# Optimization experiments

Measured on AMD Instinct MI355X. Metric: run time of the kernel, lower is better.

## Reference

```python
import jax, jax.numpy as jnp
import numpy as np

B, T, E = 2, 2048, 1024
H, D = 8, 512
ROPE_BASE = 10000.0


def apply_rope(x):
    # x: [B, H, T, D] -- rotary positional embedding, half-split convention
    t = x.shape[2]
    d = x.shape[3]
    inv_freq = 1.0 / (ROPE_BASE ** (jnp.arange(0, d, 2, dtype=jnp.float32) / d))  # [D/2]
    ang = jnp.arange(t, dtype=jnp.float32)[:, None] * inv_freq[None, :]           # [T, D/2]
    cos = jnp.cos(ang)[None, None].astype(x.dtype)
    sin = jnp.sin(ang)[None, None].astype(x.dtype)
    x1, x2 = jnp.split(x, 2, axis=-1)
    return jnp.concatenate([x1 * cos - x2 * sin, x1 * sin + x2 * cos], axis=-1)


def setup_inputs() -> dict:
    key = jax.random.key(0)
    ks = jax.random.split(key, 5)
    s_in = 1.0 / np.sqrt(E)
    s_out = 1.0 / np.sqrt(H * D)
    return {
        "x": jax.random.normal(ks[0], (B, T, E), dtype=jnp.float32),
        "Wq": jax.random.normal(ks[1], (H * D, E), dtype=jnp.float32) * s_in,
        "Wk": jax.random.normal(ks[2], (H * D, E), dtype=jnp.float32) * s_in,
        "Wv": jax.random.normal(ks[3], (H * D, E), dtype=jnp.float32) * s_in,
        "Wo": jax.random.normal(ks[4], (E, H * D), dtype=jnp.float32) * s_out,
    }


def reference(x, Wq, Wk, Wv, Wo):
    b, t, e = x.shape
    # QKV projections (bias-free Linear: x @ W.T), reshape to [B, H, T, D]
    q = (x @ Wq.T).reshape(b, t, H, D).transpose(0, 2, 1, 3)
    k = (x @ Wk.T).reshape(b, t, H, D).transpose(0, 2, 1, 3)
    v = (x @ Wv.T).reshape(b, t, H, D).transpose(0, 2, 1, 3)
    # RoPE on q and k
    q = apply_rope(q)
    k = apply_rope(k)
    # scaled dot-product attention with causal mask
    scale = 1.0 / jnp.sqrt(jnp.asarray(D, dtype=x.dtype))
    scores = jnp.einsum("bhqd,bhkd->bhqk", q, k) * scale
    causal = jnp.tril(jnp.ones((t, t), dtype=bool))
    scores = jnp.where(causal[None, None], scores, jnp.asarray(-jnp.inf, dtype=scores.dtype))
    probs = jax.nn.softmax(scores, axis=-1)  # explicitly materialized, as in source
    attn = jnp.einsum("bhqk,bhkd->bhqd", probs, v)
    out = attn.transpose(0, 2, 1, 3).reshape(b, t, H * D) @ Wo.T
    return out
```

## Files before the change

kernel.cpp:

```cpp
#include <hip/hip_runtime.h>


#define DEV __device__ __forceinline__

using bf16x8  = __attribute__((ext_vector_type(8))) short;
using floatx4 = __attribute__((ext_vector_type(4))) float;

#define MFMA16(a, b, c) __builtin_amdgcn_mfma_f32_16x16x32_bf16((a), (b), (c), 0, 0, 0)

#define KT_BH 1097728
#define KT_TILE 17152
#define KT_ROW 536
#define VT_BH 1310720
#define VT_TILE 20480

DEV unsigned short f2bf(float f) {
  union { float f; unsigned int u; } c; c.f = f;
  unsigned int u = c.u + 0x7FFFu + ((c.u >> 16) & 1u);
  return (unsigned short)(u >> 16);
}
DEV float bf2f(unsigned short h) {
  union { unsigned int u; float f; } c; c.u = ((unsigned int)h) << 16;
  return c.f;
}

DEV void ldsld16(const unsigned short* g, unsigned short* l) {
  __builtin_amdgcn_global_load_lds(
      (__attribute__((address_space(1))) void*)(g),
      (__attribute__((address_space(3))) void*)(l), 16, 0, 0);
}

__global__ void cast4_k(const float* __restrict__ x,  const float* __restrict__ wq,
                        const float* __restrict__ wk, const float* __restrict__ wv,
                        unsigned short* __restrict__ xb,  unsigned short* __restrict__ wqb,
                        unsigned short* __restrict__ wkb, unsigned short* __restrict__ wvb) {
  const float* s; unsigned short* d;
  switch (blockIdx.y) {
    case 0: s = x;  d = xb;  break;
    case 1: s = wq; d = wqb; break;
    case 2: s = wk; d = wkb; break;
    default: s = wv; d = wvb; break;
  }
  int i = blockIdx.x * 256 + threadIdx.x;
  float4 v = ((const float4*)s)[i];
  uint2 o;
  o.x = (unsigned int)f2bf(v.x) | ((unsigned int)f2bf(v.y) << 16);
  o.y = (unsigned int)f2bf(v.z) | ((unsigned int)f2bf(v.w) << 16);
  ((uint2*)d)[i] = o;
}

__global__ void cast1_k(const float* __restrict__ s, unsigned short* __restrict__ d) {
  int i = blockIdx.x * 256 + threadIdx.x;
  float4 v = ((const float4*)s)[i];
  uint2 o;
  o.x = (unsigned int)f2bf(v.x) | ((unsigned int)f2bf(v.y) << 16);
  o.y = (unsigned int)f2bf(v.z) | ((unsigned int)f2bf(v.w) << 16);
  ((uint2*)d)[i] = o;
}

__global__ __launch_bounds__(256) void qkv_gemm(
    const unsigned short* __restrict__ X,
    const unsigned short* __restrict__ Wq, const unsigned short* __restrict__ Wk,
    const unsigned short* __restrict__ Wv,
    unsigned short* __restrict__ Qo, unsigned short* __restrict__ Ko, unsigned short* __restrict__ Vo) {
  __shared__ __align__(16) unsigned short As[128 * 32];
  __shared__ __align__(16) unsigned short Bs[128 * 32];
  const int tid = threadIdx.x;
  const int wave = tid >> 6, lane = tid & 63, quad = lane >> 4, l16 = lane & 15;
  const int m0 = blockIdx.x * 128, n0 = blockIdx.y * 128;
  const int z = blockIdx.z;
  const unsigned short* W = (z == 0) ? Wq : (z == 1) ? Wk : Wv;
  const int wm = (wave >> 1) * 64, wn = (wave & 1) * 64;
  floatx4 acc[4][4];
#pragma unroll
  for (int i = 0; i < 4; ++i)
#pragma unroll
    for (int j = 0; j < 4; ++j) acc[i][j] = (floatx4){0.f, 0.f, 0.f, 0.f};

  const int r0 = wave * 32;
  const int lrow = lane >> 2, lchunk = (lane & 3) * 8;
  for (int k0 = 0; k0 < 1024; k0 += 32) {
    const unsigned short* ga = X + (size_t)(m0 + r0 + lrow) * 1024 + k0 + lchunk;
    const unsigned short* gb = W + (size_t)(n0 + r0 + lrow) * 1024 + k0 + lchunk;
    ldsld16(ga, As + r0 * 32);
    ldsld16(ga + (size_t)16 * 1024, As + r0 * 32 + 512);
    ldsld16(gb, Bs + r0 * 32);
    ldsld16(gb + (size_t)16 * 1024, Bs + r0 * 32 + 512);
    __syncthreads();
    bf16x8 af[4], bw[4];
#pragma unroll
    for (int i = 0; i < 4; ++i) af[i] = *(const bf16x8*)(As + (wm + i * 16 + l16) * 32 + quad * 8);
#pragma unroll
    for (int j = 0; j < 4; ++j) bw[j] = *(const bf16x8*)(Bs + (wn + j * 16 + l16) * 32 + quad * 8);
#pragma unroll
    for (int i = 0; i < 4; ++i)
#pragma unroll
      for (int j = 0; j < 4; ++j) acc[i][j] = MFMA16(af[i], bw[j], acc[i][j]);
    __syncthreads();
  }
#pragma unroll
  for (int i = 0; i < 4; ++i)
#pragma unroll
    for (int j = 0; j < 4; ++j) {
      int gn = n0 + wn + j * 16 + l16;
      int h = gn >> 9, d = gn & 511;
      int gm0 = m0 + wm + i * 16 + quad * 4;
      int b = gm0 >> 11, t0 = gm0 & 2047;
      int bh = b * 8 + h;
      if (z == 2) {
        unsigned short pk[4];
#pragma unroll
        for (int r = 0; r < 4; ++r) pk[r] = f2bf(acc[i][j][r]);
        size_t off = (size_t)bh * VT_BH + (t0 >> 5) * VT_TILE + (size_t)d * 40 + (t0 & 31);
        *(uint2*)(Vo + off) = *(uint2*)pk;
      } else if (z == 1) {
        size_t off = (size_t)bh * KT_BH + (t0 >> 5) * KT_TILE + (size_t)(t0 & 31) * KT_ROW + d;
#pragma unroll
        for (int r = 0; r < 4; ++r) Ko[off + (size_t)r * KT_ROW] = f2bf(acc[i][j][r]);
      } else {
        size_t base = ((size_t)(bh * 2048 + t0)) * 512 + d;
#pragma unroll
        for (int r = 0; r < 4; ++r) Qo[base + (size_t)r * 512] = f2bf(acc[i][j][r]);
      }
    }
}

__global__ void rope_k(unsigned short* __restrict__ Q, unsigned short* __restrict__ Kt) {
  int idx = blockIdx.x * 256 + threadIdx.x;
  int r = idx & 8388607;
  int row = r >> 8;
  int i = r & 255;
  int t = row & 2047;
  unsigned short* P;
  size_t base;
  if (idx & 8388608) {
    int bh = row >> 11;
    base = (size_t)bh * KT_BH + (t >> 5) * KT_TILE + (size_t)(t & 31) * KT_ROW;
    P = Kt;
  } else {
    base = (size_t)row * 512;
    P = Q;
  }
  float x1 = bf2f(P[base + i]);
  float x2 = bf2f(P[base + i + 256]);
  float freq = expf(-(float)i * 0.03597789207803197f);
  float ang = (float)t * freq;
  float sv, cv;
  sincosf(ang, &sv, &cv);
  P[base + i]       = f2bf(x1 * cv - x2 * sv);
  P[base + i + 256] = f2bf(x1 * sv + x2 * cv);
}

__global__ __launch_bounds__(256, 2) void flash_attn(
    const unsigned short* __restrict__ Q, const unsigned short* __restrict__ Kt,
    const unsigned short* __restrict__ Vt, unsigned short* __restrict__ attn,
    unsigned short* __restrict__ P1, float* __restrict__ ml1, float* __restrict__ ml2,
    int split) {
  __shared__ __align__(16) unsigned short Ks[32 * 536];
  __shared__ __align__(16) unsigned short Vs[512 * 40];
  __shared__ __align__(16) unsigned short Ps[4 * 16 * 40];
  const int tid = threadIdx.x;
  const int wave = tid >> 6, lane = tid & 63, quad = lane >> 4, l16 = lane & 15;
  const int bh = blockIdx.x, b = bh >> 3, head = bh & 7;
  const int y = blockIdx.y;
  int qi, st0, stN, om;
  if (split) {
    if (y < 16)      { qi = 31 - y; st0 = 0;  stN = 32;         om = 1; }
    else if (y < 32) { qi = 47 - y; st0 = 32; stN = 2 * qi + 2; om = 2; }
    else             { qi = 47 - y; st0 = 0;  stN = 2 * qi + 2; om = 0; }
  } else { qi = (y < 16) ? (31 - y) : (y - 16); st0 = 0; stN = 2 * qi + 2; om = 0; }

  const unsigned short* Qp = Q + ((size_t)bh << 20);
  const unsigned short* Kp = Kt + (size_t)bh * KT_BH;
  const unsigned short* Vp = Vt + (size_t)bh * VT_BH;
  const int qb = qi * 64;

  bf16x8 qf[16];
  {
    const unsigned short* qrow = Qp + (size_t)(qb + wave * 16 + l16) * 512 + quad * 8;
#pragma unroll
    for (int ks = 0; ks < 16; ++ks) qf[ks] = *(const bf16x8*)(qrow + ks * 32);
  }
  floatx4 o[32];
#pragma unroll
  for (int n = 0; n < 32; ++n) o[n] = (floatx4){0.f, 0.f, 0.f, 0.f};
  float m_[4], l_[4];
#pragma unroll
  for (int r = 0; r < 4; ++r) { m_[r] = -3.0e38f; l_[r] = 0.f; }

  unsigned short* psw = Ps + wave * 640;

  {
    const unsigned short* gk = Kp + (size_t)st0 * KT_TILE;
    const unsigned short* gv = Vp + (size_t)st0 * VT_TILE;
#pragma unroll
    for (int j = 0; j < 9; ++j) {
      int c0 = wave * 536 + j * 64;
      if (j < 8 || lane < 24) ldsld16(gk + (size_t)(c0 + lane) * 8, Ks + c0 * 8);
    }
#pragma unroll
    for (int j = 0; j < 10; ++j) {
      int c0 = wave * 640 + j * 64;
      ldsld16(gv + (size_t)(c0 + lane) * 8, Vs + c0 * 8);
    }
  }

  for (int st = st0; st < stN; ++st) {
    __syncthreads();
    const int s0 = st * 32;
    floatx4 sc0 = (floatx4){0.f, 0.f, 0.f, 0.f}, sc1 = sc0;
#pragma unroll
    for (int ks = 0; ks < 16; ++ks) {
      bf16x8 k0 = *(const bf16x8*)(Ks + (size_t)l16 * 536 + ks * 32 + quad * 8);
      bf16x8 k1 = *(const bf16x8*)(Ks + (size_t)(16 + l16) * 536 + ks * 32 + quad * 8);
      sc0 = MFMA16(qf[ks], k0, sc0);
      sc1 = MFMA16(qf[ks], k1, sc1);
    }
    const float scale = 0.04419417382415922f;
    const int qrow0 = qb + wave * 16 + quad * 4;
    float pv0[4], pv1[4], mr[4];
#pragma unroll
    for (int r = 0; r < 4; ++r) {
      float a0 = sc0[r] * scale, a1 = sc1[r] * scale;
      if (s0 + l16 > qrow0 + r) a0 = -3.0e38f;
      if (s0 + 16 + l16 > qrow0 + r) a1 = -3.0e38f;
      pv0[r] = a0; pv1[r] = a1;
      mr[r] = fmaxf(a0, a1);
    }
#pragma unroll
    for (int off = 1; off < 16; off <<= 1)
#pragma unroll
      for (int r = 0; r < 4; ++r) mr[r] = fmaxf(mr[r], __shfl_xor(mr[r], off, 64));
    float alpha[4], rs[4];
#pragma unroll
    for (int r = 0; r < 4; ++r) {
      float mn = fmaxf(m_[r], mr[r]);
      alpha[r] = __expf(m_[r] - mn);
      m_[r] = mn;
      float p0 = __expf(pv0[r] - mn);
      float p1 = __expf(pv1[r] - mn);
      rs[r] = p0 + p1;
      psw[(quad * 4 + r) * 40 + l16] = f2bf(p0);
      psw[(quad * 4 + r) * 40 + 16 + l16] = f2bf(p1);
    }
#pragma unroll
    for (int off = 1; off < 16; off <<= 1)
#pragma unroll
      for (int r = 0; r < 4; ++r) rs[r] += __shfl_xor(rs[r], off, 64);
#pragma unroll
    for (int r = 0; r < 4; ++r) l_[r] = l_[r] * alpha[r] + rs[r];
    if (__any(alpha[0] + alpha[1] + alpha[2] + alpha[3] < 4.0f)) {
#pragma unroll
      for (int n = 0; n < 32; ++n)
#pragma unroll
        for (int r = 0; r < 4; ++r) o[n][r] *= alpha[r];
    }
    bf16x8 pf = *(const bf16x8*)(psw + (size_t)l16 * 40 + quad * 8);
#pragma unroll
    for (int nt = 0; nt < 32; ++nt) {
      bf16x8 vf = *(const bf16x8*)(Vs + (size_t)(nt * 16 + l16) * 40 + quad * 8);
      o[nt] = MFMA16(pf, vf, o[nt]);
    }
    __syncthreads();
    if (st + 1 < stN) {
      const unsigned short* gk = Kp + (size_t)(st + 1) * KT_TILE;
      const unsigned short* gv = Vp + (size_t)(st + 1) * VT_TILE;
#pragma unroll
      for (int j = 0; j < 9; ++j) {
        int c0 = wave * 536 + j * 64;
        if (j < 8 || lane < 24) ldsld16(gk + (size_t)(c0 + lane) * 8, Ks + c0 * 8);
      }
#pragma unroll
      for (int j = 0; j < 10; ++j) {
        int c0 = wave * 640 + j * 64;
        ldsld16(gv + (size_t)(c0 + lane) * 8, Vs + c0 * 8);
      }
    }
  }
  const int rowi = wave * 16 + quad * 4;
  if (om == 0) {
    float inv[4];
#pragma unroll
    for (int r = 0; r < 4; ++r) inv[r] = 1.0f / l_[r];
    unsigned short* arow = attn + ((size_t)(b * 2048 + qb + rowi)) * 4096 + head * 512 + l16;
#pragma unroll
    for (int nt = 0; nt < 32; ++nt)
#pragma unroll
      for (int r = 0; r < 4; ++r)
        arow[(size_t)r * 4096 + nt * 16] = f2bf(o[nt][r] * inv[r]);
  } else {
    const int p = bh * 16 + (qi - 16);
    float* ml = (om == 1) ? ml1 : ml2;
    if (l16 == 0) {
#pragma unroll
      for (int r = 0; r < 4; ++r) {
        ml[(size_t)p * 128 + (rowi + r) * 2]     = m_[r];
        ml[(size_t)p * 128 + (rowi + r) * 2 + 1] = l_[r];
      }
    }
    if (om == 1) {
      unsigned short* prow = P1 + ((size_t)p * 64 + rowi) * 512 + l16;
#pragma unroll
      for (int nt = 0; nt < 32; ++nt)
#pragma unroll
        for (int r = 0; r < 4; ++r)
          prow[(size_t)r * 512 + nt * 16] = f2bf(o[nt][r]);
    } else {
      unsigned short* arow = attn + ((size_t)(b * 2048 + qb + rowi)) * 4096 + head * 512 + l16;
#pragma unroll
      for (int nt = 0; nt < 32; ++nt)
#pragma unroll
        for (int r = 0; r < 4; ++r)
          arow[(size_t)r * 4096 + nt * 16] = f2bf(o[nt][r]);
    }
  }
}

__global__ void combine_k(const unsigned short* __restrict__ P1,
                          const float* __restrict__ ml1, const float* __restrict__ ml2,
                          unsigned short* __restrict__ attn) {
  const int p = blockIdx.x;
  const int bh = p >> 4, b = bh >> 3, head = bh & 7, qi = 16 + (p & 15);
  const int tid = threadIdx.x;
#pragma unroll
  for (int it = 0; it < 16; ++it) {
    int idx = it * 256 + tid;
    int row = idx >> 6, c8 = (idx & 63) * 8;
    float m1 = ml1[(size_t)p * 128 + row * 2], l1 = ml1[(size_t)p * 128 + row * 2 + 1];
    float m2 = ml2[(size_t)p * 128 + row * 2], l2 = ml2[(size_t)p * 128 + row * 2 + 1];
    float M = fmaxf(m1, m2);
    float w1 = __expf(m1 - M), w2 = __expf(m2 - M);
    float inv = 1.0f / (l1 * w1 + l2 * w2);
    const unsigned short* o1 = P1 + ((size_t)p * 64 + row) * 512 + c8;
    unsigned short* ap = attn + ((size_t)(b * 2048 + qi * 64 + row)) * 4096 + head * 512 + c8;
    unsigned short res[8];
#pragma unroll
    for (int j = 0; j < 8; ++j)
      res[j] = f2bf((bf2f(o1[j]) * w1 + bf2f(ap[j]) * w2) * inv);
    *(bf16x8*)ap = *(bf16x8*)res;
  }
}

__global__ __launch_bounds__(256) void out_gemm(
    const unsigned short* __restrict__ A, const unsigned short* __restrict__ W,
    float* __restrict__ C) {
  __shared__ __align__(16) unsigned short As[128 * 32];
  __shared__ __align__(16) unsigned short Bs[128 * 32];
  const int tid = threadIdx.x;
  const int wave = tid >> 6, lane = tid & 63, quad = lane >> 4, l16 = lane & 15;
  const int m0 = blockIdx.x * 128, n0 = blockIdx.y * 128;
  const int kb = blockIdx.z * 1024;
  const int wm = (wave >> 1) * 64, wn = (wave & 1) * 64;
  floatx4 acc[4][4];
#pragma unroll
  for (int i = 0; i < 4; ++i)
#pragma unroll
    for (int j = 0; j < 4; ++j) acc[i][j] = (floatx4){0.f, 0.f, 0.f, 0.f};
  const int r0 = wave * 32;
  const int lrow = lane >> 2, lchunk = (lane & 3) * 8;
  for (int k0 = kb; k0 < kb + 1024; k0 += 32) {
    const unsigned short* ga = A + (size_t)(m0 + r0 + lrow) * 4096 + k0 + lchunk;
    const unsigned short* gb = W + (size_t)(n0 + r0 + lrow) * 4096 + k0 + lchunk;
    ldsld16(ga, As + r0 * 32);
    ldsld16(ga + (size_t)16 * 4096, As + r0 * 32 + 512);
    ldsld16(gb, Bs + r0 * 32);
    ldsld16(gb + (size_t)16 * 4096, Bs + r0 * 32 + 512);
    __syncthreads();
    bf16x8 af[4], bw[4];
#pragma unroll
    for (int i = 0; i < 4; ++i) af[i] = *(const bf16x8*)(As + (wm + i * 16 + l16) * 32 + quad * 8);
#pragma unroll
    for (int j = 0; j < 4; ++j) bw[j] = *(const bf16x8*)(Bs + (wn + j * 16 + l16) * 32 + quad * 8);
#pragma unroll
    for (int i = 0; i < 4; ++i)
#pragma unroll
      for (int j = 0; j < 4; ++j) acc[i][j] = MFMA16(af[i], bw[j], acc[i][j]);
    __syncthreads();
  }
#pragma unroll
  for (int i = 0; i < 4; ++i)
#pragma unroll
    for (int j = 0; j < 4; ++j) {
      int gn = n0 + wn + j * 16 + l16;
#pragma unroll
      for (int r = 0; r < 4; ++r) {
        int gm = m0 + wm + i * 16 + quad * 4 + r;
        unsafeAtomicAdd(&C[(size_t)gm * 1024 + gn], acc[i][j][r]);
      }
    }
}

extern "C" void kernel_launch(void* const* d_in, const int* in_sizes, int n_in,
                              void* d_out, int out_size, void* d_ws, size_t ws_size,
                              hipStream_t stream) {
  const float* x  = (const float*)d_in[0];
  const float* Wq = (const float*)d_in[1];
  const float* Wk = (const float*)d_in[2];
  const float* Wv = (const float*)d_in[3];
  const float* Wo = (const float*)d_in[4];
  float* out = (float*)d_out;
  char* ws = (char*)d_ws;
  const size_t MB = 1048576;
  unsigned short* xb    = (unsigned short*)(ws + 0 * MB);
  unsigned short* wqb   = (unsigned short*)(ws + 8 * MB);
  unsigned short* wkb   = (unsigned short*)(ws + 16 * MB);
  unsigned short* wvb   = (unsigned short*)(ws + 24 * MB);
  unsigned short* attnb = (unsigned short*)(ws + 0 * MB);
  unsigned short* Qb    = (unsigned short*)(ws + 32 * MB);
  unsigned short* wob   = (unsigned short*)(ws + 32 * MB);
  unsigned short* Ktb   = (unsigned short*)(ws + 64 * MB);
  unsigned short* Vtb   = (unsigned short*)(ws + 98 * MB);
  unsigned short* P1    = (unsigned short*)(ws + 138 * MB);
  float* ml1            = (float*)(ws + 154 * MB);
  float* ml2            = (float*)(ws + 154 * MB + 131072);
  const int split = (ws_size >= (size_t)160 * MB) ? 1 : 0;

  hipMemsetAsync(d_out, 0, (size_t)4096 * 1024 * 4, stream);

  cast4_k<<<dim3(4096, 4), 256, 0, stream>>>(x, Wq, Wk, Wv, xb, wqb, wkb, wvb);
  qkv_gemm<<<dim3(32, 32, 3), 256, 0, stream>>>(xb, wqb, wkb, wvb, Qb, Ktb, Vtb);
  rope_k<<<65536, 256, 0, stream>>>(Qb, Ktb);
  flash_attn<<<dim3(16, split ? 48 : 32), 256, 0, stream>>>(Qb, Ktb, Vtb, attnb, P1, ml1, ml2, split);
  if (split) combine_k<<<256, 256, 0, stream>>>(P1, ml1, ml2, attnb);
  cast1_k<<<4096, 256, 0, stream>>>(Wo, wob);
  out_gemm<<<dim3(32, 8, 4), 256, 0, stream>>>(attnb, wob, out);
}
```

Measured before the change: 702.2 us.

## Double-buffer K/V tiles in flash attention with 8-wave 128-row query blocks

The flash attention kernel moves from 4 waves with 64 query rows per block to 8 waves with 128 rows. The K and V tiles staged in shared memory are now double-buffered, so the next tile loads while the current one is being computed, and one barrier per step is dropped. The split-K schedule and the combine kernel are redone for the larger query blocks, with fewer blocks overall and only the six largest query blocks split in two. The LDS footprint roughly doubles, which together with the doubled thread count may limit occupancy, and the coarser grid gives fewer blocks to balance the causal triangle.

```diff
diff --git a/kernel.cpp b/kernel.cpp
--- a/kernel.cpp
+++ b/kernel.cpp
@@ -151,33 +151,39 @@
   P[base + i + 256] = f2bf(x1 * sv + x2 * cv);
 }
 
-__global__ __launch_bounds__(256, 2) void flash_attn(
+__global__ __launch_bounds__(512, 2) void flash_attn(
     const unsigned short* __restrict__ Q, const unsigned short* __restrict__ Kt,
     const unsigned short* __restrict__ Vt, unsigned short* __restrict__ attn,
     unsigned short* __restrict__ P1, float* __restrict__ ml1, float* __restrict__ ml2,
     int split) {
-  __shared__ __align__(16) unsigned short Ks[32 * 536];
-  __shared__ __align__(16) unsigned short Vs[512 * 40];
-  __shared__ __align__(16) unsigned short Ps[4 * 16 * 40];
+  __shared__ __align__(16) unsigned short Ks[2 * 32 * 536];
+  __shared__ __align__(16) unsigned short Vs[2 * 512 * 40];
+  __shared__ __align__(16) unsigned short Ps[8 * 16 * 40];
   const int tid = threadIdx.x;
   const int wave = tid >> 6, lane = tid & 63, quad = lane >> 4, l16 = lane & 15;
   const int bh = blockIdx.x, b = bh >> 3, head = bh & 7;
   const int y = blockIdx.y;
-  int qi, st0, stN, om;
+  int qi, st0 = 0, stN, om = 0;
   if (split) {
-    if (y < 16)      { qi = 31 - y; st0 = 0;  stN = 32;         om = 1; }
-    else if (y < 32) { qi = 47 - y; st0 = 32; stN = 2 * qi + 2; om = 2; }
-    else             { qi = 47 - y; st0 = 0;  stN = 2 * qi + 2; om = 0; }
-  } else { qi = (y < 16) ? (31 - y) : (y - 16); st0 = 0; stN = 2 * qi + 2; om = 0; }
+    if (y == 0)      { qi = 9; stN = 4 * qi + 4; }
+    else if (y == 1) { qi = 8; stN = 4 * qi + 4; }
+    else if (y < 14) {
+      qi = 15 - ((y - 2) >> 1);
+      int mid = 2 * qi + 2;
+      if ((y & 1) == 0) { st0 = 0;   stN = mid;        om = 1; }
+      else              { st0 = mid; stN = 4 * qi + 4; om = 2; }
+    } else { qi = 7 - (y - 14); stN = 4 * qi + 4; }
+  } else { qi = 15 - y; stN = 4 * qi + 4; }
 
   const unsigned short* Qp = Q + ((size_t)bh << 20);
   const unsigned short* Kp = Kt + (size_t)bh * KT_BH;
   const unsigned short* Vp = Vt + (size_t)bh * VT_BH;
-  const int qb = qi * 64;
+  const int qb = qi * 128;
+  const int qw0 = qb + wave * 16;
 
   bf16x8 qf[16];
   {
-    const unsigned short* qrow = Qp + (size_t)(qb + wave * 16 + l16) * 512 + quad * 8;
+    const unsigned short* qrow = Qp + (size_t)(qw0 + l16) * 512 + quad * 8;
 #pragma unroll
     for (int ks = 0; ks < 16; ++ks) qf[ks] = *(const bf16x8*)(qrow + ks * 32);
   }
@@ -189,35 +195,51 @@
   for (int r = 0; r < 4; ++r) { m_[r] = -3.0e38f; l_[r] = 0.f; }
 
   unsigned short* psw = Ps + wave * 640;
+  const int kc0 = wave * 268;
+  const int vc0 = wave * 320;
 
   {
     const unsigned short* gk = Kp + (size_t)st0 * KT_TILE;
     const unsigned short* gv = Vp + (size_t)st0 * VT_TILE;
 #pragma unroll
-    for (int j = 0; j < 9; ++j) {
-      int c0 = wave * 536 + j * 64;
-      if (j < 8 || lane < 24) ldsld16(gk + (size_t)(c0 + lane) * 8, Ks + c0 * 8);
-    }
-#pragma unroll
-    for (int j = 0; j < 10; ++j) {
-      int c0 = wave * 640 + j * 64;
-      ldsld16(gv + (size_t)(c0 + lane) * 8, Vs + c0 * 8);
-    }
+    for (int j = 0; j < 4; ++j)
+      ldsld16(gk + (size_t)(kc0 + j * 64 + lane) * 8, Ks + (kc0 + j * 64) * 8);
+    if (lane < 12) ldsld16(gk + (size_t)(kc0 + 256 + lane) * 8, Ks + (kc0 + 256) * 8);
+#pragma unroll
+    for (int j = 0; j < 5; ++j)
+      ldsld16(gv + (size_t)(vc0 + j * 64 + lane) * 8, Vs + (vc0 + j * 64) * 8);
   }
 
   for (int st = st0; st < stN; ++st) {
+    const int cur = (st - st0) & 1;
     __syncthreads();
+    if (st + 1 < stN) {
+      const int nxt = cur ^ 1;
+      const unsigned short* gk = Kp + (size_t)(st + 1) * KT_TILE;
+      const unsigned short* gv = Vp + (size_t)(st + 1) * VT_TILE;
+      unsigned short* kd = Ks + nxt * 17152;
+      unsigned short* vd = Vs + nxt * 20480;
+#pragma unroll
+      for (int j = 0; j < 4; ++j)
+        ldsld16(gk + (size_t)(kc0 + j * 64 + lane) * 8, kd + (kc0 + j * 64) * 8);
+      if (lane < 12) ldsld16(gk + (size_t)(kc0 + 256 + lane) * 8, kd + (kc0 + 256) * 8);
+#pragma unroll
+      for (int j = 0; j < 5; ++j)
+        ldsld16(gv + (size_t)(vc0 + j * 64 + lane) * 8, vd + (vc0 + j * 64) * 8);
+    }
+    const unsigned short* ksb = Ks + cur * 17152;
+    const unsigned short* vsb = Vs + cur * 20480;
     const int s0 = st * 32;
     floatx4 sc0 = (floatx4){0.f, 0.f, 0.f, 0.f}, sc1 = sc0;
 #pragma unroll
     for (int ks = 0; ks < 16; ++ks) {
-      bf16x8 k0 = *(const bf16x8*)(Ks + (size_t)l16 * 536 + ks * 32 + quad * 8);
-      bf16x8 k1 = *(const bf16x8*)(Ks + (size_t)(16 + l16) * 536 + ks * 32 + quad * 8);
+      bf16x8 k0 = *(const bf16x8*)(ksb + (size_t)l16 * 536 + ks * 32 + quad * 8);
+      bf16x8 k1 = *(const bf16x8*)(ksb + (size_t)(16 + l16) * 536 + ks * 32 + quad * 8);
       sc0 = MFMA16(qf[ks], k0, sc0);
       sc1 = MFMA16(qf[ks], k1, sc1);
     }
     const float scale = 0.04419417382415922f;
-    const int qrow0 = qb + wave * 16 + quad * 4;
+    const int qrow0 = qw0 + quad * 4;
     float pv0[4], pv1[4], mr[4];
 #pragma unroll
     for (int r = 0; r < 4; ++r) {
@@ -258,23 +280,8 @@
     bf16x8 pf = *(const bf16x8*)(psw + (size_t)l16 * 40 + quad * 8);
 #pragma unroll
     for (int nt = 0; nt < 32; ++nt) {
-      bf16x8 vf = *(const bf16x8*)(Vs + (size_t)(nt * 16 + l16) * 40 + quad * 8);
+      bf16x8 vf = *(const bf16x8*)(vsb + (size_t)(nt * 16 + l16) * 40 + quad * 8);
       o[nt] = MFMA16(pf, vf, o[nt]);
-    }
-    __syncthreads();
-    if (st + 1 < stN) {
-      const unsigned short* gk = Kp + (size_t)(st + 1) * KT_TILE;
-      const unsigned short* gv = Vp + (size_t)(st + 1) * VT_TILE;
-#pragma unroll
-      for (int j = 0; j < 9; ++j) {
-        int c0 = wave * 536 + j * 64;
-        if (j < 8 || lane < 24) ldsld16(gk + (size_t)(c0 + lane) * 8, Ks + c0 * 8);
-      }
-#pragma unroll
-      for (int j = 0; j < 10; ++j) {
-        int c0 = wave * 640 + j * 64;
-        ldsld16(gv + (size_t)(c0 + lane) * 8, Vs + c0 * 8);
-      }
     }
   }
   const int rowi = wave * 16 + quad * 4;
@@ -289,17 +296,17 @@
       for (int r = 0; r < 4; ++r)
         arow[(size_t)r * 4096 + nt * 16] = f2bf(o[nt][r] * inv[r]);
   } else {
-    const int p = bh * 16 + (qi - 16);
+    const int p = bh * 6 + (qi - 10);
     float* ml = (om == 1) ? ml1 : ml2;
     if (l16 == 0) {
 #pragma unroll
       for (int r = 0; r < 4; ++r) {
-        ml[(size_t)p * 128 + (rowi + r) * 2]     = m_[r];
-        ml[(size_t)p * 128 + (rowi + r) * 2 + 1] = l_[r];
+        ml[(size_t)p * 256 + (rowi + r) * 2]     = m_[r];
+        ml[(size_t)p * 256 + (rowi + r) * 2 + 1] = l_[r];
       }
     }
     if (om == 1) {
-      unsigned short* prow = P1 + ((size_t)p * 64 + rowi) * 512 + l16;
+      unsigned short* prow = P1 + ((size_t)p * 128 + rowi) * 512 + l16;
 #pragma unroll
       for (int nt = 0; nt < 32; ++nt)
 #pragma unroll
@@ -320,19 +327,20 @@
                           const float* __restrict__ ml1, const float* __restrict__ ml2,
                           unsigned short* __restrict__ attn) {
   const int p = blockIdx.x;
-  const int bh = p >> 4, b = bh >> 3, head = bh & 7, qi = 16 + (p & 15);
+  const int bh = p / 6, qi = 10 + (p - bh * 6);
+  const int b = bh >> 3, head = bh & 7;
   const int tid = threadIdx.x;
 #pragma unroll
-  for (int it = 0; it < 16; ++it) {
+  for (int it = 0; it < 32; ++it) {
     int idx = it * 256 + tid;
     int row = idx >> 6, c8 = (idx & 63) * 8;
-    float m1 = ml1[(size_t)p * 128 + row * 2], l1 = ml1[(size_t)p * 128 + row * 2 + 1];
-    float m2 = ml2[(size_t)p * 128 + row * 2], l2 = ml2[(size_t)p * 128 + row * 2 + 1];
+    float m1 = ml1[(size_t)p * 256 + row * 2], l1 = ml1[(size_t)p * 256 + row * 2 + 1];
+    float m2 = ml2[(size_t)p * 256 + row * 2], l2 = ml2[(size_t)p * 256 + row * 2 + 1];
     float M = fmaxf(m1, m2);
     float w1 = __expf(m1 - M), w2 = __expf(m2 - M);
     float inv = 1.0f / (l1 * w1 + l2 * w2);
-    const unsigned short* o1 = P1 + ((size_t)p * 64 + row) * 512 + c8;
-    unsigned short* ap = attn + ((size_t)(b * 2048 + qi * 64 + row)) * 4096 + head * 512 + c8;
+    const unsigned short* o1 = P1 + ((size_t)p * 128 + row) * 512 + c8;
+    unsigned short* ap = attn + ((size_t)(b * 2048 + qi * 128 + row)) * 4096 + head * 512 + c8;
     unsigned short res[8];
 #pragma unroll
     for (int j = 0; j < 8; ++j)
@@ -420,8 +428,8 @@
   cast4_k<<<dim3(4096, 4), 256, 0, stream>>>(x, Wq, Wk, Wv, xb, wqb, wkb, wvb);
   qkv_gemm<<<dim3(32, 32, 3), 256, 0, stream>>>(xb, wqb, wkb, wvb, Qb, Ktb, Vtb);
   rope_k<<<65536, 256, 0, stream>>>(Qb, Ktb);
-  flash_attn<<<dim3(16, split ? 48 : 32), 256, 0, stream>>>(Qb, Ktb, Vtb, attnb, P1, ml1, ml2, split);
-  if (split) combine_k<<<256, 256, 0, stream>>>(P1, ml1, ml2, attnb);
+  flash_attn<<<dim3(16, split ? 22 : 16), 512, 0, stream>>>(Qb, Ktb, Vtb, attnb, P1, ml1, ml2, split);
+  if (split) combine_k<<<96, 256, 0, stream>>>(P1, ml1, ml2, attnb);
   cast1_k<<<4096, 256, 0, stream>>>(Wo, wob);
   out_gemm<<<dim3(32, 8, 4), 256, 0, stream>>>(attnb, wob, out);
 }
```

Result: faster. 613.2 us (-12.7%).
